# Kernel optimization log

Hardware: AMD Instinct MI355X
Metric: run time of the kernel (lower is better)

The kernel has to match this reference:

```python
import jax, jax.numpy as jnp
import numpy as np

EPS = 1e-5

def _layer_norm(x, gamma, beta):
    mu = jnp.mean(x, axis=-1, keepdims=True)
    var = jnp.mean(jnp.square(x - mu), axis=-1, keepdims=True)
    return (x - mu) * jax.lax.rsqrt(var + EPS) * gamma + beta

def setup_inputs() -> dict:
    key = jax.random.key(0)
    ks = jax.random.split(key, 4)
    B, S, D, F = 4, 2048, 1024, 4096
    return {
        "hidden_state": jax.random.normal(ks[0], (B, S, D), dtype=jnp.float32),
        "attention_mask": jnp.zeros((B, S), dtype=jnp.float32),
        "w1": jax.random.normal(ks[1], (D, F), dtype=jnp.float32) * (1.0 / np.sqrt(D)),
        "b1": jnp.zeros((F,), dtype=jnp.float32),
        "w2": jax.random.normal(ks[2], (F, D), dtype=jnp.float32) * (1.0 / np.sqrt(F)),
        "b2": jnp.zeros((D,), dtype=jnp.float32),
        "ln1_gamma": jnp.ones((D,), dtype=jnp.float32),
        "ln1_beta": jnp.zeros((D,), dtype=jnp.float32),
        "ln2_gamma": jnp.ones((D,), dtype=jnp.float32),
        "ln2_beta": jnp.zeros((D,), dtype=jnp.float32),
    }

def reference(hidden_state, attention_mask, w1, b1, w2, b2,
              ln1_gamma, ln1_beta, ln2_gamma, ln2_beta):
    h = hidden_state
    d = h.shape[-1]
    # Self-attention with Q=K=V=h (no projections), single head.
    scores = jnp.einsum("bqd,bkd->bqk", h, h) / jnp.sqrt(jnp.float32(d))
    scores = scores + attention_mask[:, None, :]  # additive mask [B,1,S]
    probs = jax.nn.softmax(scores, axis=-1)
    attn_out = jnp.einsum("bqk,bkd->bqd", probs, h)
    # Residual + post-LN (dropout inactive in eval)
    h = _layer_norm(h + attn_out, ln1_gamma, ln1_beta)
    # FFN: Linear -> exact GELU -> Linear
    ffn = jax.nn.gelu(h @ w1 + b1, approximate=False) @ w2 + b2
    h = _layer_norm(h + ffn, ln2_gamma, ln2_beta)
    return h
```

## Files before the change

### kernel.cpp

```cpp
#include <hip/hip_runtime.h>
#include <hip/hip_bf16.h>
#include <math.h>

typedef __bf16 bf16;
typedef __bf16 bf16x8 __attribute__((ext_vector_type(8)));
typedef float  f32x4  __attribute__((ext_vector_type(4)));

__device__ __forceinline__ float gelu_f(float x) {
    return 0.5f * x * (1.0f + erff(x * 0.70710678118654752440f));
}

__global__ void detect_k(const unsigned short* __restrict__ h, int* __restrict__ flag)
{
    if (threadIdx.x == 0 && blockIdx.x == 0) {
        int cnt = 0;
        for (int i = 0; i < 256; i += 2) {
            int e = (h[i] >> 7) & 0xFF;
            cnt += (e >= 100 && e <= 140) ? 1 : 0;
        }
        *flag = (cnt >= 96) ? 0 : 1;
    }
}

struct SmallConvArgs {
    const void* src[7];
    bf16* dst[7];
    int n[7];
};
__global__ __launch_bounds__(256) void small_convert_k(SmallConvArgs a,
                                                       const int* __restrict__ flag)
{
    const int seg = blockIdx.y;
    const int i = blockIdx.x * 256 + threadIdx.x;
    if (i >= a.n[seg]) return;
    const float v = (*flag) ? ((const float*)a.src[seg])[i]
                            : (float)((const bf16*)a.src[seg])[i];
    a.dst[seg][i] = (bf16)v;
}

__global__ __launch_bounds__(256) void conv_transpose_k(
    const void* __restrict__ in, bf16* __restrict__ outT,
    int R, int C, const int* __restrict__ flag)
{
    __shared__ bf16 tile[32][33];
    const int c0 = blockIdx.x * 32;
    const int r0 = blockIdx.y * 32;
    const int tx = threadIdx.x & 31;
    const int ty = threadIdx.x >> 5;
    const bool f32 = (*flag) != 0;
#pragma unroll
    for (int i = 0; i < 32; i += 8) {
        const long idx = (long)(r0 + ty + i) * C + (c0 + tx);
        const float v = f32 ? ((const float*)in)[idx] : (float)((const bf16*)in)[idx];
        tile[ty + i][tx] = (bf16)v;
    }
    __syncthreads();
#pragma unroll
    for (int i = 0; i < 32; i += 8)
        outT[(long)(c0 + ty + i) * R + (r0 + tx)] = tile[tx][ty + i];
}

__global__ __launch_bounds__(256) void conv_transpose_h_k(
    const void* __restrict__ in, bf16* __restrict__ h_bf, bf16* __restrict__ hT,
    int S, int D, const int* __restrict__ flag)
{
    __shared__ bf16 tile[32][33];
    const long sB = (long)S * D;
    const int d0 = blockIdx.x * 32;
    const int s0 = blockIdx.y * 32;
    const int b  = blockIdx.z;
    const int tx = threadIdx.x & 31;
    const int ty = threadIdx.x >> 5;
    const bool f32 = (*flag) != 0;
#pragma unroll
    for (int i = 0; i < 32; i += 8) {
        const long idx = b * sB + (long)(s0 + ty + i) * D + (d0 + tx);
        const float v = f32 ? ((const float*)in)[idx] : (float)((const bf16*)in)[idx];
        const bf16 bv = (bf16)v;
        h_bf[idx] = bv;
        tile[ty + i][tx] = bv;
    }
    __syncthreads();
#pragma unroll
    for (int i = 0; i < 32; i += 8)
        hT[b * sB + (long)(d0 + ty + i) * S + (s0 + tx)] = tile[tx][ty + i];
}

template <int MODE>
__global__ __launch_bounds__(256) void gemm_nt(
    const bf16* __restrict__ A, const bf16* __restrict__ Bt,
    bf16* __restrict__ C, const bf16* __restrict__ bias,
    int M, int N, int K, float scale,
    long sA, long sB, long sC)
{
    A  += (long)blockIdx.z * sA;
    Bt += (long)blockIdx.z * sB;
    C  += (long)blockIdx.z * sC;

    const int tileM = blockIdx.y * 128;
    const int tileN = blockIdx.x * 128;

    __shared__ __align__(16) bf16 As[128 * 64];
    __shared__ __align__(16) bf16 Bs[128 * 64];

    const int t    = threadIdx.x;
    const int lane = t & 63;
    const int wave = t >> 6;
    const int wr   = wave >> 1;
    const int wc   = wave & 1;
    const int quad = lane >> 4;
    const int l16  = lane & 15;

    f32x4 acc[4][4] = {};

    auto swz = [](int row, int chunk) { return row * 64 + (((chunk + row) & 7) * 8); };

    for (int k0 = 0; k0 < K; k0 += 64) {
        bf16x8 ra[4], rb[4];
#pragma unroll
        for (int r = 0; r < 4; ++r) {
            const int e   = (r * 256 + t) * 8;
            const int row = e >> 6;
            const int col = e & 63;
            ra[r] = *(const bf16x8*)(A  + (long)(tileM + row) * K + (k0 + col));
            rb[r] = *(const bf16x8*)(Bt + (long)(tileN + row) * K + (k0 + col));
        }
#pragma unroll
        for (int r = 0; r < 4; ++r) {
            const int row = (r * 256 + t) >> 3;
            const int off = swz(row, t & 7);
            *(bf16x8*)&As[off] = ra[r];
            *(bf16x8*)&Bs[off] = rb[r];
        }
        __syncthreads();

#pragma unroll
        for (int kk = 0; kk < 64; kk += 32) {
            const int chunk = (kk >> 3) + quad;
            bf16x8 af[4], bfr[4];
#pragma unroll
            for (int i = 0; i < 4; ++i) {
                af[i]  = *(const bf16x8*)&As[swz(wr * 64 + i * 16 + l16, chunk)];
                bfr[i] = *(const bf16x8*)&Bs[swz(wc * 64 + i * 16 + l16, chunk)];
            }
#pragma unroll
            for (int mi = 0; mi < 4; ++mi)
#pragma unroll
                for (int ni = 0; ni < 4; ++ni)
                    acc[mi][ni] = __builtin_amdgcn_mfma_f32_16x16x32_bf16(
                        af[mi], bfr[ni], acc[mi][ni], 0, 0, 0);
        }
        __syncthreads();
    }

#pragma unroll
    for (int mi = 0; mi < 4; ++mi) {
        const int rbase = tileM + wr * 64 + mi * 16 + quad * 4;
#pragma unroll
        for (int ni = 0; ni < 4; ++ni) {
            const int col = tileN + wc * 64 + ni * 16 + l16;
            float bv = 0.0f;
            if (MODE >= 2) bv = (float)bias[col];
#pragma unroll
            for (int r = 0; r < 4; ++r) {
                float v = acc[mi][ni][r];
                if (MODE == 0) v *= scale;
                if (MODE >= 2) v += bv;
                if (MODE == 2) v = gelu_f(v);
                C[(long)(rbase + r) * N + col] = (bf16)v;
            }
        }
    }
}

__global__ __launch_bounds__(256) void softmax_k(
    bf16* __restrict__ scores, const bf16* __restrict__ mask, int S)
{
    const long rowOff = ((long)blockIdx.y * S + blockIdx.x) * S;
    bf16* row = scores + rowOff;
    const bf16* mrow = mask + (long)blockIdx.y * S;
    const int t = threadIdx.x;

    const bf16x8 r = ((const bf16x8*)row)[t];
    const bf16x8 m = ((const bf16x8*)mrow)[t];
    float v[8];
    float mx = -1e30f;
#pragma unroll
    for (int i = 0; i < 8; ++i) {
        v[i] = (float)r[i] + (float)m[i];
        mx = fmaxf(mx, v[i]);
    }
#pragma unroll
    for (int off = 32; off > 0; off >>= 1)
        mx = fmaxf(mx, __shfl_down(mx, off));
    __shared__ float redm[4];
    if ((t & 63) == 0) redm[t >> 6] = mx;
    __syncthreads();
    mx = fmaxf(fmaxf(redm[0], redm[1]), fmaxf(redm[2], redm[3]));

    float s = 0.0f;
#pragma unroll
    for (int i = 0; i < 8; ++i) { v[i] = __expf(v[i] - mx); s += v[i]; }
#pragma unroll
    for (int off = 32; off > 0; off >>= 1)
        s += __shfl_down(s, off);
    __shared__ float reds[4];
    if ((t & 63) == 0) reds[t >> 6] = s;
    __syncthreads();
    s = reds[0] + reds[1] + reds[2] + reds[3];
    const float inv = 1.0f / s;
    bf16x8 o;
#pragma unroll
    for (int i = 0; i < 8; ++i) o[i] = (bf16)(v[i] * inv);
    ((bf16x8*)row)[t] = o;
}

__global__ __launch_bounds__(128) void ln_residual_k(
    const bf16* __restrict__ x1, const bf16* __restrict__ x2,
    const bf16* __restrict__ gamma, const bf16* __restrict__ beta,
    bf16* __restrict__ out)
{
    constexpr int D = 1024;
    const long off = (long)blockIdx.x * D;
    const int t = threadIdx.x;
    const bf16x8 a = ((const bf16x8*)(x1 + off))[t];
    const bf16x8 b = ((const bf16x8*)(x2 + off))[t];
    float v[8];
    float s = 0.0f, s2 = 0.0f;
#pragma unroll
    for (int i = 0; i < 8; ++i) {
        v[i] = (float)a[i] + (float)b[i];
        s  += v[i];
        s2 += v[i] * v[i];
    }
#pragma unroll
    for (int o2 = 32; o2 > 0; o2 >>= 1) {
        s  += __shfl_down(s, o2);
        s2 += __shfl_down(s2, o2);
    }
    __shared__ float rs[2], rs2[2];
    if ((t & 63) == 0) { rs[t >> 6] = s; rs2[t >> 6] = s2; }
    __syncthreads();
    s  = rs[0] + rs[1];
    s2 = rs2[0] + rs2[1];
    const float mean = s / (float)D;
    const float var  = s2 / (float)D - mean * mean;
    const float inv  = rsqrtf(var + 1e-5f);
    const bf16x8 g  = ((const bf16x8*)gamma)[t];
    const bf16x8 be = ((const bf16x8*)beta)[t];
    bf16x8 o;
#pragma unroll
    for (int i = 0; i < 8; ++i)
        o[i] = (bf16)((v[i] - mean) * inv * (float)g[i] + (float)be[i]);
    ((bf16x8*)(out + off))[t] = o;
}

__global__ __launch_bounds__(128) void ln_out_k(
    const bf16* __restrict__ x1, const bf16* __restrict__ x2,
    const bf16* __restrict__ gamma, const bf16* __restrict__ beta,
    void* __restrict__ outv, const int* __restrict__ flag)
{
    constexpr int D = 1024;
    const long off = (long)blockIdx.x * D;
    const int t = threadIdx.x;
    const bf16x8 a = ((const bf16x8*)(x1 + off))[t];
    const bf16x8 b = ((const bf16x8*)(x2 + off))[t];
    float v[8];
    float s = 0.0f, s2 = 0.0f;
#pragma unroll
    for (int i = 0; i < 8; ++i) {
        v[i] = (float)a[i] + (float)b[i];
        s  += v[i];
        s2 += v[i] * v[i];
    }
#pragma unroll
    for (int o2 = 32; o2 > 0; o2 >>= 1) {
        s  += __shfl_down(s, o2);
        s2 += __shfl_down(s2, o2);
    }
    __shared__ float rs[2], rs2[2];
    if ((t & 63) == 0) { rs[t >> 6] = s; rs2[t >> 6] = s2; }
    __syncthreads();
    s  = rs[0] + rs[1];
    s2 = rs2[0] + rs2[1];
    const float mean = s / (float)D;
    const float var  = s2 / (float)D - mean * mean;
    const float inv  = rsqrtf(var + 1e-5f);
    const bf16x8 g  = ((const bf16x8*)gamma)[t];
    const bf16x8 be = ((const bf16x8*)beta)[t];
    if (*flag) {
        f32x4 o1, o2v;
#pragma unroll
        for (int i = 0; i < 4; ++i) {
            o1[i]  = (v[i] - mean) * inv * (float)g[i] + (float)be[i];
            o2v[i] = (v[4 + i] - mean) * inv * (float)g[4 + i] + (float)be[4 + i];
        }
        f32x4* op = (f32x4*)((float*)outv + off);
        op[t * 2]     = o1;
        op[t * 2 + 1] = o2v;
    } else {
        bf16x8 o;
#pragma unroll
        for (int i = 0; i < 8; ++i)
            o[i] = (bf16)((v[i] - mean) * inv * (float)g[i] + (float)be[i]);
        ((bf16x8*)((bf16*)outv + off))[t] = o;
    }
}

extern "C" void kernel_launch(void* const* d_in, const int* in_sizes, int n_in,
                              void* d_out, int out_size, void* d_ws, size_t ws_size,
                              hipStream_t stream)
{
    constexpr int B = 4, S = 2048, D = 1024, F = 4096;
    constexpr long MB = 1024 * 1024;

    const void* h_raw  = d_in[0];
    const void* mk_raw = d_in[1];
    const void* w1_raw = d_in[2];
    const void* b1_raw = d_in[3];
    const void* w2_raw = d_in[4];
    const void* b2_raw = d_in[5];
    const void* g1_raw = d_in[6];
    const void* be1_raw= d_in[7];
    const void* g2_raw = d_in[8];
    const void* be2_raw= d_in[9];

    char* ws = (char*)d_ws;
    bf16* scores = (bf16*)(ws + 0);
    bf16* gact   = (bf16*)(ws + 0);
    bf16* hT     = (bf16*)(ws + 32 * MB);
    bf16* h_bf   = (bf16*)(ws + 48 * MB);
    bf16* y1     = (bf16*)(ws + 64 * MB);
    bf16* w1T    = (bf16*)(ws + 80 * MB);
    bf16* w2T    = (bf16*)(ws + 88 * MB);
    bf16* axf    = (bf16*)(ws + 96 * MB);
    char* sm     = ws + 112 * MB;
    int*  flag   = (int*)(sm);
    bf16* mk_bf  = (bf16*)(sm + 1024);
    bf16* b1_bf  = (bf16*)(sm + 17408 + 1024);
    bf16* b2_bf  = (bf16*)(sm + 25600 + 3072);
    bf16* g1_bf  = (bf16*)(sm + 27648 + 3072);
    bf16* be1_bf = (bf16*)(sm + 29696 + 3072);
    bf16* g2_bf  = (bf16*)(sm + 31744 + 3072);
    bf16* be2_bf = (bf16*)(sm + 33792 + 3072);

    const long SD = (long)S * D;
    const long SS = (long)S * S;

    detect_k<<<1, 64, 0, stream>>>((const unsigned short*)h_raw, flag);

    SmallConvArgs sca;
    sca.src[0] = mk_raw;  sca.dst[0] = mk_bf;  sca.n[0] = B * S;
    sca.src[1] = b1_raw;  sca.dst[1] = b1_bf;  sca.n[1] = F;
    sca.src[2] = b2_raw;  sca.dst[2] = b2_bf;  sca.n[2] = D;
    sca.src[3] = g1_raw;  sca.dst[3] = g1_bf;  sca.n[3] = D;
    sca.src[4] = be1_raw; sca.dst[4] = be1_bf; sca.n[4] = D;
    sca.src[5] = g2_raw;  sca.dst[5] = g2_bf;  sca.n[5] = D;
    sca.src[6] = be2_raw; sca.dst[6] = be2_bf; sca.n[6] = D;
    small_convert_k<<<dim3((B * S) / 256, 7), 256, 0, stream>>>(sca, flag);

    conv_transpose_h_k<<<dim3(D / 32, S / 32, B), 256, 0, stream>>>(
        h_raw, h_bf, hT, S, D, flag);

    conv_transpose_k<<<dim3(F / 32, D / 32), 256, 0, stream>>>(w1_raw, w1T, D, F, flag);
    conv_transpose_k<<<dim3(D / 32, F / 32), 256, 0, stream>>>(w2_raw, w2T, F, D, flag);

    gemm_nt<0><<<dim3(S / 128, S / 128, B), 256, 0, stream>>>(
        h_bf, h_bf, scores, nullptr, S, S, D, 0.03125f, SD, SD, SS);

    softmax_k<<<dim3(S, B), 256, 0, stream>>>(scores, mk_bf, S);

    gemm_nt<1><<<dim3(D / 128, S / 128, B), 256, 0, stream>>>(
        scores, hT, axf, nullptr, S, D, S, 1.0f, SS, SD, SD);

    ln_residual_k<<<B * S, 128, 0, stream>>>(h_bf, axf, g1_bf, be1_bf, y1);

    gemm_nt<2><<<dim3(F / 128, (B * S) / 128, 1), 256, 0, stream>>>(
        y1, w1T, gact, b1_bf, B * S, F, D, 1.0f, 0, 0, 0);

    gemm_nt<3><<<dim3(D / 128, (B * S) / 128, 1), 256, 0, stream>>>(
        gact, w2T, axf, b2_bf, B * S, D, F, 1.0f, 0, 0, 0);

    ln_out_k<<<B * S, 128, 0, stream>>>(y1, axf, g2_bf, be2_bf, d_out, flag);
}
```

Before: 476.6 us.

## Add 256x256 double-buffered GEMM with direct global-to-LDS loads for QK and FFN1

Adds a new GEMM kernel with 256x256 tiles and 512 threads that double-buffers LDS. Tiles are staged with global_load_lds so global data goes straight into shared memory, and loads for the next k-steps are interleaved with MFMA phases under s_setprio. The QK^T scores GEMM and the first FFN GEMM now use it. The aim is more data reuse per tile and hidden memory latency, at the cost of 128KB LDS per block and fewer blocks for smaller grids.

Result: slower. 487.6 us (+2.3%).

```diff
diff --git a/kernel.cpp b/kernel.cpp
--- a/kernel.cpp
+++ b/kernel.cpp
@@ -86,6 +86,13 @@
         hT[b * sB + (long)(d0 + ty + i) * S + (s0 + tx)] = tile[tx][ty + i];
 }
 
+__device__ __forceinline__ void gll16(const bf16* g, bf16* l)
+{
+    __builtin_amdgcn_global_load_lds(
+        (const __attribute__((address_space(1))) void*)g,
+        (__attribute__((address_space(3))) void*)l, 16, 0, 0);
+}
+
 template <int MODE>
 __global__ __launch_bounds__(256) void gemm_nt(
     const bf16* __restrict__ A, const bf16* __restrict__ Bt,
@@ -156,6 +163,175 @@
 #pragma unroll
     for (int mi = 0; mi < 4; ++mi) {
         const int rbase = tileM + wr * 64 + mi * 16 + quad * 4;
+#pragma unroll
+        for (int ni = 0; ni < 4; ++ni) {
+            const int col = tileN + wc * 64 + ni * 16 + l16;
+            float bv = 0.0f;
+            if (MODE >= 2) bv = (float)bias[col];
+#pragma unroll
+            for (int r = 0; r < 4; ++r) {
+                float v = acc[mi][ni][r];
+                if (MODE == 0) v *= scale;
+                if (MODE >= 2) v += bv;
+                if (MODE == 2) v = gelu_f(v);
+                C[(long)(rbase + r) * N + col] = (bf16)v;
+            }
+        }
+    }
+}
+
+template <int MODE>
+__global__ __launch_bounds__(512, 2) void gemm_nt_256(
+    const bf16* __restrict__ A, const bf16* __restrict__ Bt,
+    bf16* __restrict__ C, const bf16* __restrict__ bias,
+    int M, int N, int K, float scale,
+    long sA, long sB, long sC)
+{
+    A  += (long)blockIdx.z * sA;
+    Bt += (long)blockIdx.z * sB;
+    C  += (long)blockIdx.z * sC;
+
+    const int tileM = blockIdx.y * 256;
+    const int tileN = blockIdx.x * 256;
+
+    __shared__ __align__(16) bf16 As[2][256 * 64];
+    __shared__ __align__(16) bf16 Bs[2][256 * 64];
+
+    const int t    = threadIdx.x;
+    const int lane = t & 63;
+    const int wave = t >> 6;
+    const int wr   = wave >> 2;
+    const int wc   = wave & 3;
+    const int quad = lane >> 4;
+    const int l16  = lane & 15;
+
+    const int srow   = lane >> 3;
+    const int lchunk = ((lane & 7) - srow) & 7;
+
+    const int NK = K >> 6;
+
+    auto stageHalf = [&](const bf16* src, bf16* lbuf, int rowBase, int k0) {
+#pragma unroll
+        for (int rnd = 0; rnd < 2; ++rnd) {
+            const int r = rnd * 64 + wave * 8;
+            const bf16* g = src + (long)(rowBase + r + srow) * K + (k0 + lchunk * 8);
+            gll16(g, lbuf + r * 64);
+        }
+    };
+
+    auto swz = [](int row, int chunk) { return row * 64 + (((chunk + row) & 7) * 8); };
+
+    f32x4 acc[8][4] = {};
+
+    stageHalf(Bt, &Bs[0][0],        tileN,       0);
+    stageHalf(Bt, &Bs[0][128 * 64], tileN + 128, 0);
+    stageHalf(A,  &As[0][0],        tileM,       0);
+    stageHalf(A,  &As[0][128 * 64], tileM + 128, 0);
+    if (NK > 1) {
+        stageHalf(Bt, &Bs[1][0], tileN, 64);
+        stageHalf(A,  &As[1][0], tileM, 64);
+        asm volatile("s_waitcnt vmcnt(4)" ::: "memory");
+    } else {
+        asm volatile("s_waitcnt vmcnt(0)" ::: "memory");
+    }
+    __builtin_amdgcn_s_barrier();
+
+    for (int u = 0; u < NK; ++u) {
+        const int cu = u & 1;
+        const int nx = cu ^ 1;
+        const bf16* asb = &As[cu][0];
+        const bf16* bsb = &Bs[cu][0];
+        const int k1 = (u + 1) << 6;
+        const int k2 = (u + 2) << 6;
+        const bool st1 = (u + 1 < NK);
+        const bool st2 = (u + 2 < NK);
+
+        bf16x8 aF[4][2], bF[4][2];
+
+#pragma unroll
+        for (int mi = 0; mi < 4; ++mi)
+#pragma unroll
+            for (int ks = 0; ks < 2; ++ks)
+                aF[mi][ks] = *(const bf16x8*)&asb[swz(wr * 128 + mi * 16 + l16, ks * 4 + quad)];
+#pragma unroll
+        for (int ni = 0; ni < 2; ++ni)
+#pragma unroll
+            for (int ks = 0; ks < 2; ++ks)
+                bF[ni][ks] = *(const bf16x8*)&bsb[swz(wc * 64 + ni * 16 + l16, ks * 4 + quad)];
+        if (st1) stageHalf(Bt, &Bs[nx][128 * 64], tileN + 128, k1);
+        __builtin_amdgcn_s_barrier();
+        __builtin_amdgcn_s_setprio(1);
+#pragma unroll
+        for (int mi = 0; mi < 4; ++mi)
+#pragma unroll
+            for (int ni = 0; ni < 2; ++ni)
+#pragma unroll
+                for (int ks = 0; ks < 2; ++ks)
+                    acc[mi][ni] = __builtin_amdgcn_mfma_f32_16x16x32_bf16(
+                        aF[mi][ks], bF[ni][ks], acc[mi][ni], 0, 0, 0);
+        __builtin_amdgcn_s_setprio(0);
+        __builtin_amdgcn_s_barrier();
+
+#pragma unroll
+        for (int ni = 0; ni < 2; ++ni)
+#pragma unroll
+            for (int ks = 0; ks < 2; ++ks)
+                bF[2 + ni][ks] = *(const bf16x8*)&bsb[swz(wc * 64 + (2 + ni) * 16 + l16, ks * 4 + quad)];
+        if (st1) stageHalf(A, &As[nx][128 * 64], tileM + 128, k1);
+        __builtin_amdgcn_s_barrier();
+        __builtin_amdgcn_s_setprio(1);
+#pragma unroll
+        for (int mi = 0; mi < 4; ++mi)
+#pragma unroll
+            for (int ni = 0; ni < 2; ++ni)
+#pragma unroll
+                for (int ks = 0; ks < 2; ++ks)
+                    acc[mi][2 + ni] = __builtin_amdgcn_mfma_f32_16x16x32_bf16(
+                        aF[mi][ks], bF[2 + ni][ks], acc[mi][2 + ni], 0, 0, 0);
+        __builtin_amdgcn_s_setprio(0);
+        __builtin_amdgcn_s_barrier();
+
+#pragma unroll
+        for (int mi = 0; mi < 4; ++mi)
+#pragma unroll
+            for (int ks = 0; ks < 2; ++ks)
+                aF[mi][ks] = *(const bf16x8*)&asb[swz(wr * 128 + (4 + mi) * 16 + l16, ks * 4 + quad)];
+        if (st2) stageHalf(Bt, &Bs[cu][0], tileN, k2);
+        __builtin_amdgcn_s_barrier();
+        __builtin_amdgcn_s_setprio(1);
+#pragma unroll
+        for (int mi = 0; mi < 4; ++mi)
+#pragma unroll
+            for (int ni = 0; ni < 2; ++ni)
+#pragma unroll
+                for (int ks = 0; ks < 2; ++ks)
+                    acc[4 + mi][ni] = __builtin_amdgcn_mfma_f32_16x16x32_bf16(
+                        aF[mi][ks], bF[ni][ks], acc[4 + mi][ni], 0, 0, 0);
+        __builtin_amdgcn_s_setprio(0);
+        __builtin_amdgcn_s_barrier();
+
+        if (st2) stageHalf(A, &As[cu][0], tileM, k2);
+        __builtin_amdgcn_s_setprio(1);
+#pragma unroll
+        for (int mi = 0; mi < 4; ++mi)
+#pragma unroll
+            for (int ni = 0; ni < 2; ++ni)
+#pragma unroll
+                for (int ks = 0; ks < 2; ++ks)
+                    acc[4 + mi][2 + ni] = __builtin_amdgcn_mfma_f32_16x16x32_bf16(
+                        aF[mi][ks], bF[2 + ni][ks], acc[4 + mi][2 + ni], 0, 0, 0);
+        __builtin_amdgcn_s_setprio(0);
+
+        if (st1) {
+            if (st2) asm volatile("s_waitcnt vmcnt(4)" ::: "memory");
+            else     asm volatile("s_waitcnt vmcnt(0)" ::: "memory");
+            __builtin_amdgcn_s_barrier();
+        }
+    }
+
+#pragma unroll
+    for (int mi = 0; mi < 8; ++mi) {
+        const int rbase = tileM + wr * 128 + mi * 16 + quad * 4;
 #pragma unroll
         for (int ni = 0; ni < 4; ++ni) {
             const int col = tileN + wc * 64 + ni * 16 + l16;
@@ -365,7 +541,7 @@
     conv_transpose_k<<<dim3(F / 32, D / 32), 256, 0, stream>>>(w1_raw, w1T, D, F, flag);
     conv_transpose_k<<<dim3(D / 32, F / 32), 256, 0, stream>>>(w2_raw, w2T, F, D, flag);
 
-    gemm_nt<0><<<dim3(S / 128, S / 128, B), 256, 0, stream>>>(
+    gemm_nt_256<0><<<dim3(S / 256, S / 256, B), 512, 0, stream>>>(
         h_bf, h_bf, scores, nullptr, S, S, D, 0.03125f, SD, SD, SS);
 
     softmax_k<<<dim3(S, B), 256, 0, stream>>>(scores, mk_bf, S);
@@ -375,7 +551,7 @@
 
     ln_residual_k<<<B * S, 128, 0, stream>>>(h_bf, axf, g1_bf, be1_bf, y1);
 
-    gemm_nt<2><<<dim3(F / 128, (B * S) / 128, 1), 256, 0, stream>>>(
+    gemm_nt_256<2><<<dim3(F / 256, (B * S) / 256, 1), 512, 0, stream>>>(
         y1, w1T, gact, b1_bf, B * S, F, D, 1.0f, 0, 0, 0);
 
     gemm_nt<3><<<dim3(D / 128, (B * S) / 128, 1), 256, 0, stream>>>(
```
